# Optimization experiments

Hardware: AMD Instinct MI355X
Metric: run time of the kernel (lower is better)

The kernel has to match this reference:

```python
import jax, jax.numpy as jnp
import numpy as np

B, T, S = 4, 4096, 4096
D_MODEL = 512        # d_query = d_value_in = d_key_in
N_HEADS = 8
D_KEY = 512
D_VALUE = 512
N_OMEGA = 64
EPS = 1e-9
DK_H = D_KEY // N_HEADS      # 64
DV_H = D_VALUE // N_HEADS    # 64


def _glorot(key, shape):
    fan_in, fan_out = shape[-2], shape[-1]
    lim = np.sqrt(6.0 / (fan_in + fan_out))
    return jax.random.uniform(key, shape, jnp.float32, -lim, lim)


def _draw_omega(key, d_feature, n_omega):
    # n_omega == d_feature here -> single orthogonal block scaled by sqrt(d)
    g = jax.random.normal(key, (d_feature, d_feature), jnp.float32)
    q, _ = jnp.linalg.qr(g)
    q = q * jnp.sqrt(jnp.float32(d_feature))
    return q[:n_omega]


def setup_inputs() -> dict:
    key = jax.random.key(0)
    ks = jax.random.split(key, 7)
    return {
        "query": 0.5 * jax.random.normal(ks[0], (B, T, D_MODEL), jnp.float32),
        "value": 0.5 * jax.random.normal(ks[1], (B, S, D_MODEL), jnp.float32),
        "key": 0.5 * jax.random.normal(ks[2], (B, S, D_MODEL), jnp.float32),
        "wq": _glorot(ks[3], (N_HEADS, D_MODEL, DK_H)),
        "wv": _glorot(ks[4], (N_HEADS, D_MODEL, DV_H)),
        "wk": _glorot(ks[5], (N_HEADS, D_MODEL, DK_H)),
        "omega": _draw_omega(ks[6], DK_H, N_OMEGA),
    }


def _phi(x, omega):
    # x: (B,H,T,dk_h) -> (B,H,T,2*n_omega) FAVOR+ positive random features
    square_sum = 0.5 * jnp.sum(x * x, axis=-1, keepdims=True)
    xw = jnp.einsum('bhtk,mk->bhtm', x, omega)
    un = jnp.exp(jnp.concatenate([xw, -xw], axis=-1) - square_sum) + EPS
    return un / jnp.sqrt(jnp.float32(2.0 * N_OMEGA))


def reference(query, value, key, wq, wv, wk, omega):
    q = jnp.einsum('btf,hfk->bhtk', query, wq)   # (B,H,T,dk_h)
    v = jnp.einsum('bsd,hdk->bhsk', value, wv)   # (B,H,S,dv_h)
    k = jnp.einsum('bsf,hfk->bhsk', key, wk)     # (B,H,S,dk_h)
    qp = _phi(q, omega)                          # (B,H,T,2M)
    kp = _phi(k, omega)                          # (B,H,S,2M)
    v1 = jnp.concatenate([v, jnp.ones(v.shape[:-1] + (1,), v.dtype)], axis=-1)
    kv = jnp.einsum('bhsm,bhsd->bhmd', kp, v1)   # (B,H,2M,dv_h+1)
    qkv = jnp.einsum('bhtm,bhmd->bhtd', qp, kv)  # (B,H,T,dv_h+1)
    normalizer = qkv[..., -1:]
    out = qkv[..., :-1] / normalizer
    # faithful to original: plain reshape (B,H,T,dv_h) -> (B,T,D_VALUE), no transpose
    return jnp.reshape(out, (B, T, D_VALUE))
```

## Files before the change

### kernel.cpp

```cpp
#include <hip/hip_runtime.h>

typedef _Float16 half8 __attribute__((ext_vector_type(8)));
typedef _Float16 half4_t __attribute__((ext_vector_type(4)));
typedef short short8 __attribute__((ext_vector_type(8)));
typedef unsigned short u16x4 __attribute__((ext_vector_type(4)));
typedef float f32x4 __attribute__((ext_vector_type(4)));

#define NH 8

__device__ __forceinline__ unsigned short f2bf(float x) {
  union { float f; unsigned u; } v; v.f = x;
  unsigned r = v.u + 0x7FFFu + ((v.u >> 16) & 1u);
  return (unsigned short)(r >> 16);
}

#define DRAIN_BAR()                                  \
  asm volatile("s_waitcnt lgkmcnt(0)" ::: "memory"); \
  __builtin_amdgcn_s_barrier();                      \
  __builtin_amdgcn_sched_barrier(0)

__global__ __launch_bounds__(256) void k0_qk(
    const float* __restrict__ wq, const float* __restrict__ wk,
    const float* __restrict__ omega,
    _Float16* __restrict__ wxq, _Float16* __restrict__ wxk) {
  const int bid = blockIdx.x;
  const int arr = bid >> 7;
  const int h = (bid >> 4) & 7;
  const int ft = (bid >> 1) & 7;
  const int os = bid & 1;
  const int f = threadIdx.x & 63;
  const int w = threadIdx.x >> 6;
  const float* wsrc = (arr ? wk : wq) + ((size_t)h * 512 + ft * 64 + f) * 64;
  float wreg[64];
#pragma unroll
  for (int i = 0; i < 16; ++i) {
    float4 v = *(const float4*)(wsrc + i * 4);
    wreg[i * 4] = v.x; wreg[i * 4 + 1] = v.y; wreg[i * 4 + 2] = v.z; wreg[i * 4 + 3] = v.w;
  }
  _Float16* outp = arr ? wxk : wxq;
  const int k8 = f >> 3, e = f & 7;
#pragma unroll 1
  for (int oo = 0; oo < 8; ++oo) {
    const int o = w * 16 + os * 8 + oo;
    const float* om = omega + o * 64;
    float s = 0.f;
#pragma unroll
    for (int k = 0; k < 64; ++k) s = fmaf(wreg[k], om[k], s);
    outp[((((size_t)h * 8 + ft) * 8 + k8) * 64 + o) * 8 + e] = (_Float16)s;
  }
}

__global__ __launch_bounds__(256) void k0_v(
    const float* __restrict__ wv, _Float16* __restrict__ wvt) {
  int idx = blockIdx.x * 256 + threadIdx.x;
  int h = idx >> 15, o = (idx >> 9) & 63, f = idx & 511;
  float val = wv[((size_t)h * 512 + f) * 64 + o];
  wvt[((((size_t)h * 8 + (f >> 6)) * 8 + ((f >> 3) & 7)) * 64 + o) * 8 + (f & 7)] = (_Float16)val;
}

__global__ __launch_bounds__(512, 1) void fused_kv(
    const float* __restrict__ key, const float* __restrict__ value,
    const _Float16* __restrict__ wxk, const _Float16* __restrict__ wvt,
    float* __restrict__ kvpart) {
  __shared__ __align__(16) _Float16 A[2][128][72];
  __shared__ __align__(16) _Float16 W[2][2][4096];
  __shared__ __align__(16) unsigned short kpT[128][136];
  __shared__ __align__(16) unsigned short vT[64][136];
  const int bid = blockIdx.x;
  const int hp = bid >> 6;
  const int b = (bid >> 4) & 3;
  const int sc = bid & 15;
  const int s0 = sc * 256;
  const int tid = threadIdx.x;
  const int w = tid >> 6;
  const int lane = tid & 63;
  const int g = lane >> 4, c = lane & 15;
  const int hh = w >> 2;
  const int rq = w & 3;
  const int xr = lane >> 4;
  const int xc = (lane & 15) * 4;

  const _Float16* wkb0 = wxk + (size_t)(hp * 2) * 32768;
  const _Float16* wkb1 = wkb0 + 32768;
  const _Float16* wvb0 = wvt + (size_t)(hp * 2) * 32768;
  const _Float16* wvb1 = wvb0 + 32768;

  short8 bones;
#pragma unroll
  for (int i = 0; i < 8; ++i) bones[i] = (c == 0) ? (short)0x3F80 : (short)0;

  f32x4 acc_kv[2][5];
#pragma unroll
  for (int h2 = 0; h2 < 2; ++h2)
#pragma unroll
    for (int j = 0; j < 5; ++j) acc_kv[h2][j] = (f32x4){0.f, 0.f, 0.f, 0.f};

  u16x4 kps[2][4], kms[2][4], vs_[2][4];

  float4 xv[4];
  half8 wr0, wr1;

#pragma unroll 1
  for (int p = 0; p < 4; ++p) {
    const float* xb = ((p & 1) ? value : key) +
                      (size_t)(b * 4096 + s0 + (p >> 1) * 128 + w * 16 + xr) * 512 + xc;
    const _Float16* wb0 = (p & 1) ? wvb0 : wkb0;
    const _Float16* wb1 = (p & 1) ? wvb1 : wkb1;

#pragma unroll
    for (int i = 0; i < 4; ++i) xv[i] = *(const float4*)(xb + i * 2048);
    wr0 = *(const half8*)(wb0 + tid * 8);
    wr1 = *(const half8*)(wb1 + tid * 8);
#pragma unroll
    for (int i = 0; i < 4; ++i) {
      float vv[4] = {xv[i].x, xv[i].y, xv[i].z, xv[i].w};
      half4_t hv;
#pragma unroll
      for (int j2 = 0; j2 < 4; ++j2) hv[j2] = (_Float16)vv[j2];
      *(half4_t*)&A[0][w * 16 + i * 4 + xr][xc] = hv;
    }
    *(half8*)&W[0][0][tid * 8] = wr0;
    *(half8*)&W[0][1][tid * 8] = wr1;
#pragma unroll
    for (int i = 0; i < 4; ++i) xv[i] = *(const float4*)(xb + 64 + i * 2048);
    wr0 = *(const half8*)(wb0 + 4096 + tid * 8);
    wr1 = *(const half8*)(wb1 + 4096 + tid * 8);
    DRAIN_BAR();

    f32x4 accp[2][4];
#pragma unroll
    for (int mf = 0; mf < 2; ++mf)
#pragma unroll
      for (int j = 0; j < 4; ++j) accp[mf][j] = (f32x4){0.f, 0.f, 0.f, 0.f};

#pragma unroll 1
    for (int kc = 0; kc < 8; ++kc) {
      const int cur = kc & 1;
      if (kc < 7) {
        const int nxt = cur ^ 1;
#pragma unroll
        for (int i = 0; i < 4; ++i) {
          float vv[4] = {xv[i].x, xv[i].y, xv[i].z, xv[i].w};
          half4_t hv;
#pragma unroll
          for (int j2 = 0; j2 < 4; ++j2) hv[j2] = (_Float16)vv[j2];
          *(half4_t*)&A[nxt][w * 16 + i * 4 + xr][xc] = hv;
        }
        *(half8*)&W[nxt][0][tid * 8] = wr0;
        *(half8*)&W[nxt][1][tid * 8] = wr1;
        if (kc < 6) {
#pragma unroll
          for (int i = 0; i < 4; ++i)
            xv[i] = *(const float4*)(xb + (kc + 2) * 64 + i * 2048);
          wr0 = *(const half8*)(wb0 + (kc + 2) * 4096 + tid * 8);
          wr1 = *(const half8*)(wb1 + (kc + 2) * 4096 + tid * 8);
        }
      }
#pragma unroll
      for (int ks = 0; ks < 2; ++ks) {
        half8 af0 = *(const half8*)&A[cur][rq * 32 + c][ks * 32 + g * 8];
        half8 af1 = *(const half8*)&A[cur][rq * 32 + 16 + c][ks * 32 + g * 8];
#pragma unroll
        for (int nf = 0; nf < 4; ++nf) {
          half8 wf = *(const half8*)&W[cur][hh][((ks * 4 + g) * 64 + nf * 16 + c) * 8];
          accp[0][nf] = __builtin_amdgcn_mfma_f32_16x16x32_f16(af0, wf, accp[0][nf], 0, 0, 0);
          accp[1][nf] = __builtin_amdgcn_mfma_f32_16x16x32_f16(af1, wf, accp[1][nf], 0, 0, 0);
        }
      }
      DRAIN_BAR();
    }

    if ((p & 1) == 0) {
#pragma unroll
      for (int mf = 0; mf < 2; ++mf) {
        float ss_[4];
#pragma unroll
        for (int j = 0; j < 4; ++j) {
          float s = 0.f;
#pragma unroll
          for (int nf = 0; nf < 4; ++nf) { float q = accp[mf][nf][j]; s = fmaf(q, q, s); }
          s += __shfl_xor(s, 1); s += __shfl_xor(s, 2);
          s += __shfl_xor(s, 4); s += __shfl_xor(s, 8);
          ss_[j] = s * 0.0078125f;
        }
#pragma unroll
        for (int nf = 0; nf < 4; ++nf) {
          u16x4 kp_p, kp_m;
#pragma unroll
          for (int j = 0; j < 4; ++j) {
            float v = accp[mf][nf][j];
            kp_p[j] = f2bf(__expf(v - ss_[j]) + 1e-9f);
            kp_m[j] = f2bf(__expf(-v - ss_[j]) + 1e-9f);
          }
          kps[mf][nf] = kp_p;
          kms[mf][nf] = kp_m;
        }
      }
    } else {
#pragma unroll
      for (int mf = 0; mf < 2; ++mf)
#pragma unroll
        for (int nf = 0; nf < 4; ++nf) {
          u16x4 vv;
#pragma unroll
          for (int j = 0; j < 4; ++j) vv[j] = f2bf(accp[mf][nf][j]);
          vs_[mf][nf] = vv;
        }
#pragma unroll
      for (int h2 = 0; h2 < 2; ++h2) {
        if (hh == h2) {
#pragma unroll
          for (int mf = 0; mf < 2; ++mf)
#pragma unroll
            for (int nf = 0; nf < 4; ++nf) {
              const int m = nf * 16 + c;
              const int sl = rq * 32 + mf * 16 + g * 4;
              *(u16x4*)&kpT[m][sl] = kps[mf][nf];
              *(u16x4*)&kpT[64 + m][sl] = kms[mf][nf];
              *(u16x4*)&vT[m][sl] = vs_[mf][nf];
            }
        }
        DRAIN_BAR();
#pragma unroll
        for (int ks = 0; ks < 4; ++ks) {
          short8 a = *(const short8*)&kpT[w * 16 + c][ks * 32 + g * 8];
#pragma unroll
          for (int nf = 0; nf < 4; ++nf) {
            short8 bb = *(const short8*)&vT[nf * 16 + c][ks * 32 + g * 8];
            acc_kv[h2][nf] = __builtin_amdgcn_mfma_f32_16x16x32_bf16(a, bb, acc_kv[h2][nf], 0, 0, 0);
          }
          acc_kv[h2][4] = __builtin_amdgcn_mfma_f32_16x16x32_bf16(a, bones, acc_kv[h2][4], 0, 0, 0);
        }
        __builtin_amdgcn_s_barrier();
      }
    }
  }

#pragma unroll
  for (int h2 = 0; h2 < 2; ++h2) {
    float* pbase = kvpart + ((size_t)sc * 32 + b * 8 + hp * 2 + h2) * 10240;
#pragma unroll
    for (int nf = 0; nf < 5; ++nf)
#pragma unroll
      for (int j = 0; j < 4; ++j)
        pbase[(w * 16 + g * 4 + j) * 80 + nf * 16 + c] = acc_kv[h2][nf][j];
  }
}

__global__ __launch_bounds__(128) void k3a_denom(
    const float* __restrict__ kvpart, float* __restrict__ invbuf,
    float* __restrict__ lsc) {
  const int bh = blockIdx.x;
  const int m = threadIdx.x;
  const float* base = kvpart + (size_t)bh * 10240 + m * 80 + 64;
  float s = 0.f;
#pragma unroll
  for (int kk = 0; kk < 16; ++kk) s += base[(size_t)kk * 327680];
  invbuf[bh * 128 + m] = 1.0f / s;
  lsc[bh * 128 + m] = __logf(s);
}

__global__ __launch_bounds__(256) void k3b_reduce(
    const float* __restrict__ kvpart, const float* __restrict__ invbuf,
    _Float16* __restrict__ kvnt) {
  const int bh = blockIdx.x;
  const int e0 = blockIdx.y * 1024 + threadIdx.x * 4;
  const int m = e0 / 80;
  const int d0 = e0 - m * 80;
  const float* base = kvpart + (size_t)bh * 10240 + e0;
  f32x4 s = (f32x4){0.f, 0.f, 0.f, 0.f};
#pragma unroll
  for (int kk = 0; kk < 16; ++kk) {
    f32x4 v = *(const f32x4*)(base + (size_t)kk * 327680);
    s += v;
  }
  const float inv = invbuf[bh * 128 + m];
  const int mst = ((m & 63) << 1) | (m >> 6);
  _Float16* outb = kvnt + (size_t)bh * 10240 + mst;
#pragma unroll
  for (int j = 0; j < 4; ++j) {
    const int d = d0 + j;
    float val;
    if (d < 64) val = s[j] * inv;
    else if (d == 64) val = 1.0f;
    else val = 0.f;
    outb[d * 128] = (_Float16)val;
  }
}

__global__ __launch_bounds__(512, 1) void fused_qo(
    const float* __restrict__ query, const _Float16* __restrict__ wxq,
    const _Float16* __restrict__ kvnt, const float* __restrict__ lsc,
    float* __restrict__ out) {
  __shared__ __align__(16) _Float16 A[2][128][72];
  __shared__ __align__(16) _Float16 W[2][2][4096];
  __shared__ __align__(16) _Float16 qpT[128][136];
  const int bid = blockIdx.x;
  const int hp = bid >> 7;
  const int rt = bid & 127;
  const int b = rt >> 5;
  const int t0 = (rt & 31) * 128;
  const int tid = threadIdx.x;
  const int w = tid >> 6;
  const int lane = tid & 63;
  const int g = lane >> 4, c = lane & 15;
  const int hh = w >> 2;
  const int rq = w & 3;
  const int xr = lane >> 4;
  const int xc = (lane & 15) * 4;

  const float* xb = query + (size_t)(rt * 128 + w * 16 + xr) * 512 + xc;
  const _Float16* wb0 = wxq + (size_t)(hp * 2) * 32768;
  const _Float16* wb1 = wb0 + 32768;

  float4 xv[4];
  half8 wr0, wr1;
#pragma unroll
  for (int i = 0; i < 4; ++i) xv[i] = *(const float4*)(xb + i * 2048);
  wr0 = *(const half8*)(wb0 + tid * 8);
  wr1 = *(const half8*)(wb1 + tid * 8);
#pragma unroll
  for (int i = 0; i < 4; ++i) {
    float vv[4] = {xv[i].x, xv[i].y, xv[i].z, xv[i].w};
    half4_t hv;
#pragma unroll
    for (int j2 = 0; j2 < 4; ++j2) hv[j2] = (_Float16)vv[j2];
    *(half4_t*)&A[0][w * 16 + i * 4 + xr][xc] = hv;
  }
  *(half8*)&W[0][0][tid * 8] = wr0;
  *(half8*)&W[0][1][tid * 8] = wr1;
#pragma unroll
  for (int i = 0; i < 4; ++i) xv[i] = *(const float4*)(xb + 64 + i * 2048);
  wr0 = *(const half8*)(wb0 + 4096 + tid * 8);
  wr1 = *(const half8*)(wb1 + 4096 + tid * 8);
  DRAIN_BAR();

  f32x4 accp[2][4];
#pragma unroll
  for (int mf = 0; mf < 2; ++mf)
#pragma unroll
    for (int j = 0; j < 4; ++j) accp[mf][j] = (f32x4){0.f, 0.f, 0.f, 0.f};

#pragma unroll 1
  for (int kc = 0; kc < 8; ++kc) {
    const int cur = kc & 1;
    if (kc < 7) {
      const int nxt = cur ^ 1;
#pragma unroll
      for (int i = 0; i < 4; ++i) {
        float vv[4] = {xv[i].x, xv[i].y, xv[i].z, xv[i].w};
        half4_t hv;
#pragma unroll
        for (int j2 = 0; j2 < 4; ++j2) hv[j2] = (_Float16)vv[j2];
        *(half4_t*)&A[nxt][w * 16 + i * 4 + xr][xc] = hv;
      }
      *(half8*)&W[nxt][0][tid * 8] = wr0;
      *(half8*)&W[nxt][1][tid * 8] = wr1;
      if (kc < 6) {
#pragma unroll
        for (int i = 0; i < 4; ++i)
          xv[i] = *(const float4*)(xb + (kc + 2) * 64 + i * 2048);
        wr0 = *(const half8*)(wb0 + (kc + 2) * 4096 + tid * 8);
        wr1 = *(const half8*)(wb1 + (kc + 2) * 4096 + tid * 8);
      }
    }
#pragma unroll
    for (int ks = 0; ks < 2; ++ks) {
      half8 af0 = *(const half8*)&A[cur][rq * 32 + c][ks * 32 + g * 8];
      half8 af1 = *(const half8*)&A[cur][rq * 32 + 16 + c][ks * 32 + g * 8];
#pragma unroll
      for (int nf = 0; nf < 4; ++nf) {
        half8 wf = *(const half8*)&W[cur][hh][((ks * 4 + g) * 64 + nf * 16 + c) * 8];
        accp[0][nf] = __builtin_amdgcn_mfma_f32_16x16x32_f16(af0, wf, accp[0][nf], 0, 0, 0);
        accp[1][nf] = __builtin_amdgcn_mfma_f32_16x16x32_f16(af1, wf, accp[1][nf], 0, 0, 0);
      }
    }
    DRAIN_BAR();
  }

#pragma unroll
  for (int h2 = 0; h2 < 2; ++h2) {
    const int bh = b * 8 + hp * 2 + h2;
    if (hh == h2) {
      float Lp[4], Lm[4];
#pragma unroll
      for (int nf = 0; nf < 4; ++nf) {
        Lp[nf] = lsc[bh * 128 + nf * 16 + c];
        Lm[nf] = lsc[bh * 128 + 64 + nf * 16 + c];
      }
#pragma unroll
      for (int mf = 0; mf < 2; ++mf) {
        float ss_[4], cm_[4];
#pragma unroll
        for (int j = 0; j < 4; ++j) {
          float s = 0.f;
#pragma unroll
          for (int nf = 0; nf < 4; ++nf) { float q = accp[mf][nf][j]; s = fmaf(q, q, s); }
          s += __shfl_xor(s, 1); s += __shfl_xor(s, 2);
          s += __shfl_xor(s, 4); s += __shfl_xor(s, 8);
          ss_[j] = s * 0.0078125f;
        }
#pragma unroll
        for (int j = 0; j < 4; ++j) {
          float m0 = -1e30f;
#pragma unroll
          for (int nf = 0; nf < 4; ++nf) {
            float v = accp[mf][nf][j];
            m0 = fmaxf(m0, fmaxf(v - ss_[j] + Lp[nf], -v - ss_[j] + Lm[nf]));
            m0 = fmaxf(m0, fmaxf(Lp[nf], Lm[nf]) - 20.723265f);
          }
          m0 = fmaxf(m0, __shfl_xor(m0, 1)); m0 = fmaxf(m0, __shfl_xor(m0, 2));
          m0 = fmaxf(m0, __shfl_xor(m0, 4)); m0 = fmaxf(m0, __shfl_xor(m0, 8));
          cm_[j] = m0;
        }
#pragma unroll
        for (int nf = 0; nf < 4; ++nf) {
          const int m = nf * 16 + c;
#pragma unroll
          for (int j = 0; j < 4; ++j) {
            float v = accp[mf][nf][j];
            _Float16 pp = (_Float16)(__expf(v - ss_[j] + Lp[nf] - cm_[j]) +
                                     1e-9f * __expf(Lp[nf] - cm_[j]));
            _Float16 pm = (_Float16)(__expf(-v - ss_[j] + Lm[nf] - cm_[j]) +
                                     1e-9f * __expf(Lm[nf] - cm_[j]));
            union { unsigned u; _Float16 hhx[2]; } pk;
            pk.hhx[0] = pp; pk.hhx[1] = pm;
            *(unsigned*)&qpT[rq * 32 + mf * 16 + g * 4 + j][2 * m] = pk.u;
          }
        }
      }
    }
    DRAIN_BAR();
    f32x4 acco[5];
#pragma unroll
    for (int j = 0; j < 5; ++j) acco[j] = (f32x4){0.f, 0.f, 0.f, 0.f};
    const _Float16* kvb = kvnt + (size_t)bh * 10240;
#pragma unroll
    for (int ks = 0; ks < 4; ++ks) {
      half8 a = *(const half8*)&qpT[w * 16 + c][ks * 32 + g * 8];
#pragma unroll
      for (int nf = 0; nf < 5; ++nf) {
        half8 bb = *(const half8*)(kvb + (size_t)(nf * 16 + c) * 128 + ks * 32 + g * 8);
        acco[nf] = __builtin_amdgcn_mfma_f32_16x16x32_f16(a, bb, acco[nf], 0, 0, 0);
      }
    }
    const int tb = t0 + w * 16 + g * 4;
#pragma unroll
    for (int j = 0; j < 4; ++j) {
      float nrm = __shfl(acco[4][j], (lane & 48));
      float invn = 1.0f / nrm;
#pragma unroll
      for (int nf = 0; nf < 4; ++nf) {
        out[((size_t)bh * 4096 + tb + j) * 64 + nf * 16 + c] = acco[nf][j] * invn;
      }
    }
    __builtin_amdgcn_s_barrier();
  }
}

extern "C" void kernel_launch(void* const* d_in, const int* in_sizes, int n_in,
                              void* d_out, int out_size, void* d_ws, size_t ws_size,
                              hipStream_t stream) {
  const float* query = (const float*)d_in[0];
  const float* value = (const float*)d_in[1];
  const float* key   = (const float*)d_in[2];
  const float* wq    = (const float*)d_in[3];
  const float* wv    = (const float*)d_in[4];
  const float* wk    = (const float*)d_in[5];
  const float* omega = (const float*)d_in[6];
  float* out = (float*)d_out;
  char* ws = (char*)d_ws;

  _Float16* wxq  = (_Float16*)(ws);
  _Float16* wxk  = (_Float16*)(ws + 524288);
  _Float16* wvt  = (_Float16*)(ws + 1048576);
  float* kvpart  = (float*)(ws + 1572864);
  _Float16* kvnt = (_Float16*)(ws + 22544384);
  float* lsc     = (float*)(ws + 23199744);
  float* invbuf  = (float*)(ws + 23216128);

  k0_qk<<<256, 256, 0, stream>>>(wq, wk, omega, wxq, wxk);
  k0_v<<<1024, 256, 0, stream>>>(wv, wvt);
  fused_kv<<<256, 512, 0, stream>>>(key, value, wxk, wvt, kvpart);
  k3a_denom<<<32, 128, 0, stream>>>(kvpart, invbuf, lsc);
  k3b_reduce<<<dim3(32, 10), 256, 0, stream>>>(kvpart, invbuf, kvnt);
  fused_qo<<<512, 512, 0, stream>>>(query, wxq, kvnt, lsc, out);
}
```

Baseline: 115.8 us.

## Restructure fused_qo into smaller single-head blocks for higher occupancy

```diff
diff --git a/kernel.cpp b/kernel.cpp
--- a/kernel.cpp
+++ b/kernel.cpp
@@ -288,173 +288,141 @@
   }
 }
 
-__global__ __launch_bounds__(512, 1) void fused_qo(
+__global__ __launch_bounds__(256, 4) void fused_qo(
     const float* __restrict__ query, const _Float16* __restrict__ wxq,
     const _Float16* __restrict__ kvnt, const float* __restrict__ lsc,
     float* __restrict__ out) {
-  __shared__ __align__(16) _Float16 A[2][128][72];
-  __shared__ __align__(16) _Float16 W[2][2][4096];
-  __shared__ __align__(16) _Float16 qpT[128][136];
+  __shared__ __align__(16) _Float16 A[64][72];
+  __shared__ __align__(16) _Float16 W[4096];
+  __shared__ __align__(16) _Float16 qpT[64][136];
   const int bid = blockIdx.x;
-  const int hp = bid >> 7;
-  const int rt = bid & 127;
-  const int b = rt >> 5;
-  const int t0 = (rt & 31) * 128;
+  const int h = bid >> 8;
+  const int rt = bid & 255;
+  const int R0 = rt * 64;
+  const int b = R0 >> 12;
+  const int t0 = R0 & 4095;
+  const int bh = b * NH + h;
   const int tid = threadIdx.x;
   const int w = tid >> 6;
   const int lane = tid & 63;
   const int g = lane >> 4, c = lane & 15;
-  const int hh = w >> 2;
-  const int rq = w & 3;
-  const int xr = lane >> 4;
-  const int xc = (lane & 15) * 4;
-
-  const float* xb = query + (size_t)(rt * 128 + w * 16 + xr) * 512 + xc;
-  const _Float16* wb0 = wxq + (size_t)(hp * 2) * 32768;
-  const _Float16* wb1 = wb0 + 32768;
+  const int srow = tid >> 2;
+  const int scol = (tid & 3) * 16;
+
+  const float* xb = query + (size_t)(R0 + srow) * 512 + scol;
+  const _Float16* wb = wxq + (size_t)h * 32768;
 
   float4 xv[4];
   half8 wr0, wr1;
 #pragma unroll
-  for (int i = 0; i < 4; ++i) xv[i] = *(const float4*)(xb + i * 2048);
-  wr0 = *(const half8*)(wb0 + tid * 8);
-  wr1 = *(const half8*)(wb1 + tid * 8);
-#pragma unroll
-  for (int i = 0; i < 4; ++i) {
-    float vv[4] = {xv[i].x, xv[i].y, xv[i].z, xv[i].w};
-    half4_t hv;
-#pragma unroll
-    for (int j2 = 0; j2 < 4; ++j2) hv[j2] = (_Float16)vv[j2];
-    *(half4_t*)&A[0][w * 16 + i * 4 + xr][xc] = hv;
-  }
-  *(half8*)&W[0][0][tid * 8] = wr0;
-  *(half8*)&W[0][1][tid * 8] = wr1;
-#pragma unroll
-  for (int i = 0; i < 4; ++i) xv[i] = *(const float4*)(xb + 64 + i * 2048);
-  wr0 = *(const half8*)(wb0 + 4096 + tid * 8);
-  wr1 = *(const half8*)(wb1 + 4096 + tid * 8);
-  DRAIN_BAR();
-
-  f32x4 accp[2][4];
-#pragma unroll
-  for (int mf = 0; mf < 2; ++mf)
-#pragma unroll
-    for (int j = 0; j < 4; ++j) accp[mf][j] = (f32x4){0.f, 0.f, 0.f, 0.f};
+  for (int i = 0; i < 4; ++i) xv[i] = *(const float4*)(xb + i * 4);
+  wr0 = *(const half8*)(wb + tid * 8);
+  wr1 = *(const half8*)(wb + 2048 + tid * 8);
+
+  f32x4 accp[4];
+#pragma unroll
+  for (int j = 0; j < 4; ++j) accp[j] = (f32x4){0.f, 0.f, 0.f, 0.f};
 
 #pragma unroll 1
   for (int kc = 0; kc < 8; ++kc) {
-    const int cur = kc & 1;
+    DRAIN_BAR();
+#pragma unroll
+    for (int i = 0; i < 4; ++i) {
+      float vv[4] = {xv[i].x, xv[i].y, xv[i].z, xv[i].w};
+      half4_t hv;
+#pragma unroll
+      for (int j2 = 0; j2 < 4; ++j2) hv[j2] = (_Float16)vv[j2];
+      *(half4_t*)&A[srow][scol + i * 4] = hv;
+    }
+    *(half8*)&W[tid * 8] = wr0;
+    *(half8*)&W[2048 + tid * 8] = wr1;
     if (kc < 7) {
-      const int nxt = cur ^ 1;
-#pragma unroll
-      for (int i = 0; i < 4; ++i) {
-        float vv[4] = {xv[i].x, xv[i].y, xv[i].z, xv[i].w};
-        half4_t hv;
-#pragma unroll
-        for (int j2 = 0; j2 < 4; ++j2) hv[j2] = (_Float16)vv[j2];
-        *(half4_t*)&A[nxt][w * 16 + i * 4 + xr][xc] = hv;
+#pragma unroll
+      for (int i = 0; i < 4; ++i)
+        xv[i] = *(const float4*)(xb + (kc + 1) * 64 + i * 4);
+      wr0 = *(const half8*)(wb + (size_t)(kc + 1) * 4096 + tid * 8);
+      wr1 = *(const half8*)(wb + (size_t)(kc + 1) * 4096 + 2048 + tid * 8);
+    }
+    DRAIN_BAR();
+#pragma unroll
+    for (int ks = 0; ks < 2; ++ks) {
+      half8 a = *(const half8*)&A[w * 16 + c][ks * 32 + g * 8];
+#pragma unroll
+      for (int nf = 0; nf < 4; ++nf) {
+        half8 wf = *(const half8*)&W[((ks * 4 + g) * 64 + nf * 16 + c) * 8];
+        accp[nf] = __builtin_amdgcn_mfma_f32_16x16x32_f16(a, wf, accp[nf], 0, 0, 0);
       }
-      *(half8*)&W[nxt][0][tid * 8] = wr0;
-      *(half8*)&W[nxt][1][tid * 8] = wr1;
-      if (kc < 6) {
-#pragma unroll
-        for (int i = 0; i < 4; ++i)
-          xv[i] = *(const float4*)(xb + (kc + 2) * 64 + i * 2048);
-        wr0 = *(const half8*)(wb0 + (kc + 2) * 4096 + tid * 8);
-        wr1 = *(const half8*)(wb1 + (kc + 2) * 4096 + tid * 8);
-      }
-    }
-#pragma unroll
-    for (int ks = 0; ks < 2; ++ks) {
-      half8 af0 = *(const half8*)&A[cur][rq * 32 + c][ks * 32 + g * 8];
-      half8 af1 = *(const half8*)&A[cur][rq * 32 + 16 + c][ks * 32 + g * 8];
-#pragma unroll
-      for (int nf = 0; nf < 4; ++nf) {
-        half8 wf = *(const half8*)&W[cur][hh][((ks * 4 + g) * 64 + nf * 16 + c) * 8];
-        accp[0][nf] = __builtin_amdgcn_mfma_f32_16x16x32_f16(af0, wf, accp[0][nf], 0, 0, 0);
-        accp[1][nf] = __builtin_amdgcn_mfma_f32_16x16x32_f16(af1, wf, accp[1][nf], 0, 0, 0);
-      }
-    }
-    DRAIN_BAR();
-  }
-
-#pragma unroll
-  for (int h2 = 0; h2 < 2; ++h2) {
-    const int bh = b * 8 + hp * 2 + h2;
-    if (hh == h2) {
-      float Lp[4], Lm[4];
-#pragma unroll
-      for (int nf = 0; nf < 4; ++nf) {
-        Lp[nf] = lsc[bh * 128 + nf * 16 + c];
-        Lm[nf] = lsc[bh * 128 + 64 + nf * 16 + c];
-      }
-#pragma unroll
-      for (int mf = 0; mf < 2; ++mf) {
-        float ss_[4], cm_[4];
-#pragma unroll
-        for (int j = 0; j < 4; ++j) {
-          float s = 0.f;
-#pragma unroll
-          for (int nf = 0; nf < 4; ++nf) { float q = accp[mf][nf][j]; s = fmaf(q, q, s); }
-          s += __shfl_xor(s, 1); s += __shfl_xor(s, 2);
-          s += __shfl_xor(s, 4); s += __shfl_xor(s, 8);
-          ss_[j] = s * 0.0078125f;
-        }
-#pragma unroll
-        for (int j = 0; j < 4; ++j) {
-          float m0 = -1e30f;
-#pragma unroll
-          for (int nf = 0; nf < 4; ++nf) {
-            float v = accp[mf][nf][j];
-            m0 = fmaxf(m0, fmaxf(v - ss_[j] + Lp[nf], -v - ss_[j] + Lm[nf]));
-            m0 = fmaxf(m0, fmaxf(Lp[nf], Lm[nf]) - 20.723265f);
-          }
-          m0 = fmaxf(m0, __shfl_xor(m0, 1)); m0 = fmaxf(m0, __shfl_xor(m0, 2));
-          m0 = fmaxf(m0, __shfl_xor(m0, 4)); m0 = fmaxf(m0, __shfl_xor(m0, 8));
-          cm_[j] = m0;
-        }
-#pragma unroll
-        for (int nf = 0; nf < 4; ++nf) {
-          const int m = nf * 16 + c;
-#pragma unroll
-          for (int j = 0; j < 4; ++j) {
-            float v = accp[mf][nf][j];
-            _Float16 pp = (_Float16)(__expf(v - ss_[j] + Lp[nf] - cm_[j]) +
-                                     1e-9f * __expf(Lp[nf] - cm_[j]));
-            _Float16 pm = (_Float16)(__expf(-v - ss_[j] + Lm[nf] - cm_[j]) +
-                                     1e-9f * __expf(Lm[nf] - cm_[j]));
-            union { unsigned u; _Float16 hhx[2]; } pk;
-            pk.hhx[0] = pp; pk.hhx[1] = pm;
-            *(unsigned*)&qpT[rq * 32 + mf * 16 + g * 4 + j][2 * m] = pk.u;
-          }
-        }
-      }
-    }
-    DRAIN_BAR();
-    f32x4 acco[5];
-#pragma unroll
-    for (int j = 0; j < 5; ++j) acco[j] = (f32x4){0.f, 0.f, 0.f, 0.f};
-    const _Float16* kvb = kvnt + (size_t)bh * 10240;
-#pragma unroll
-    for (int ks = 0; ks < 4; ++ks) {
-      half8 a = *(const half8*)&qpT[w * 16 + c][ks * 32 + g * 8];
-#pragma unroll
-      for (int nf = 0; nf < 5; ++nf) {
-        half8 bb = *(const half8*)(kvb + (size_t)(nf * 16 + c) * 128 + ks * 32 + g * 8);
-        acco[nf] = __builtin_amdgcn_mfma_f32_16x16x32_f16(a, bb, acco[nf], 0, 0, 0);
-      }
-    }
-    const int tb = t0 + w * 16 + g * 4;
+    }
+  }
+
+  float Lp[4], Lm[4];
+#pragma unroll
+  for (int nf = 0; nf < 4; ++nf) {
+    Lp[nf] = lsc[bh * 128 + nf * 16 + c];
+    Lm[nf] = lsc[bh * 128 + 64 + nf * 16 + c];
+  }
+  float ss_[4], cm_[4];
+#pragma unroll
+  for (int j = 0; j < 4; ++j) {
+    float s = 0.f;
+#pragma unroll
+    for (int nf = 0; nf < 4; ++nf) { float q = accp[nf][j]; s = fmaf(q, q, s); }
+    s += __shfl_xor(s, 1); s += __shfl_xor(s, 2);
+    s += __shfl_xor(s, 4); s += __shfl_xor(s, 8);
+    ss_[j] = s * 0.0078125f;
+  }
+#pragma unroll
+  for (int j = 0; j < 4; ++j) {
+    float m0 = -1e30f;
+#pragma unroll
+    for (int nf = 0; nf < 4; ++nf) {
+      float v = accp[nf][j];
+      m0 = fmaxf(m0, fmaxf(v - ss_[j] + Lp[nf], -v - ss_[j] + Lm[nf]));
+      m0 = fmaxf(m0, fmaxf(Lp[nf], Lm[nf]) - 20.723265f);
+    }
+    m0 = fmaxf(m0, __shfl_xor(m0, 1)); m0 = fmaxf(m0, __shfl_xor(m0, 2));
+    m0 = fmaxf(m0, __shfl_xor(m0, 4)); m0 = fmaxf(m0, __shfl_xor(m0, 8));
+    cm_[j] = m0;
+  }
+#pragma unroll
+  for (int nf = 0; nf < 4; ++nf) {
+    const int m = nf * 16 + c;
 #pragma unroll
     for (int j = 0; j < 4; ++j) {
-      float nrm = __shfl(acco[4][j], (lane & 48));
-      float invn = 1.0f / nrm;
-#pragma unroll
-      for (int nf = 0; nf < 4; ++nf) {
-        out[((size_t)bh * 4096 + tb + j) * 64 + nf * 16 + c] = acco[nf][j] * invn;
-      }
-    }
-    __builtin_amdgcn_s_barrier();
+      float v = accp[nf][j];
+      _Float16 pp = (_Float16)(__expf(v - ss_[j] + Lp[nf] - cm_[j]) +
+                               1e-9f * __expf(Lp[nf] - cm_[j]));
+      _Float16 pm = (_Float16)(__expf(-v - ss_[j] + Lm[nf] - cm_[j]) +
+                               1e-9f * __expf(Lm[nf] - cm_[j]));
+      union { unsigned u; _Float16 hh[2]; } pk;
+      pk.hh[0] = pp; pk.hh[1] = pm;
+      *(unsigned*)&qpT[w * 16 + g * 4 + j][2 * m] = pk.u;
+    }
+  }
+  DRAIN_BAR();
+
+  f32x4 acco[5];
+#pragma unroll
+  for (int j = 0; j < 5; ++j) acco[j] = (f32x4){0.f, 0.f, 0.f, 0.f};
+  const _Float16* kvb = kvnt + (size_t)bh * 10240;
+#pragma unroll
+  for (int ks = 0; ks < 4; ++ks) {
+    half8 a = *(const half8*)&qpT[w * 16 + c][ks * 32 + g * 8];
+#pragma unroll
+    for (int nf = 0; nf < 5; ++nf) {
+      half8 bb = *(const half8*)(kvb + (size_t)(nf * 16 + c) * 128 + ks * 32 + g * 8);
+      acco[nf] = __builtin_amdgcn_mfma_f32_16x16x32_f16(a, bb, acco[nf], 0, 0, 0);
+    }
+  }
+  const int tb = t0 + w * 16 + g * 4;
+#pragma unroll
+  for (int j = 0; j < 4; ++j) {
+    float nrm = __shfl(acco[4][j], (lane & 48));
+    float invn = 1.0f / nrm;
+#pragma unroll
+    for (int nf = 0; nf < 4; ++nf) {
+      out[((size_t)bh * 4096 + tb + j) * 64 + nf * 16 + c] = acco[nf][j] * invn;
+    }
   }
 }
 
@@ -484,5 +452,5 @@
   fused_kv<<<256, 512, 0, stream>>>(key, value, wxk, wvt, kvpart);
   k3a_denom<<<32, 128, 0, stream>>>(kvpart, invbuf, lsc);
   k3b_reduce<<<dim3(32, 10), 256, 0, stream>>>(kvpart, invbuf, kvnt);
-  fused_qo<<<512, 512, 0, stream>>>(query, wxq, kvnt, lsc, out);
-}
+  fused_qo<<<2048, 256, 0, stream>>>(query, wxq, kvnt, lsc, out);
+}
```

Result: faster. 110.0 us (-5.0%).

## Retile fused_qo to one head per block with 256-row tiles and resident weights

Applied to the files above, without the earlier changes.

```diff
diff --git a/kernel.cpp b/kernel.cpp
--- a/kernel.cpp
+++ b/kernel.cpp
@@ -292,85 +292,79 @@
     const float* __restrict__ query, const _Float16* __restrict__ wxq,
     const _Float16* __restrict__ kvnt, const float* __restrict__ lsc,
     float* __restrict__ out) {
-  __shared__ __align__(16) _Float16 A[2][128][72];
-  __shared__ __align__(16) _Float16 W[2][2][4096];
-  __shared__ __align__(16) _Float16 qpT[128][136];
+  __shared__ __align__(16) _Float16 A[2][256][72];
+  __shared__ __align__(16) _Float16 W[8][4096];
   const int bid = blockIdx.x;
-  const int hp = bid >> 7;
-  const int rt = bid & 127;
-  const int b = rt >> 5;
-  const int t0 = (rt & 31) * 128;
+  const int h = bid >> 6;
+  const int b = (bid >> 4) & 3;
+  const int tt = bid & 15;
+  const int t0 = tt * 256;
   const int tid = threadIdx.x;
   const int w = tid >> 6;
   const int lane = tid & 63;
   const int g = lane >> 4, c = lane & 15;
-  const int hh = w >> 2;
-  const int rq = w & 3;
   const int xr = lane >> 4;
   const int xc = (lane & 15) * 4;
-
-  const float* xb = query + (size_t)(rt * 128 + w * 16 + xr) * 512 + xc;
-  const _Float16* wb0 = wxq + (size_t)(hp * 2) * 32768;
-  const _Float16* wb1 = wb0 + 32768;
-
-  float4 xv[4];
-  half8 wr0, wr1;
-#pragma unroll
-  for (int i = 0; i < 4; ++i) xv[i] = *(const float4*)(xb + i * 2048);
-  wr0 = *(const half8*)(wb0 + tid * 8);
-  wr1 = *(const half8*)(wb1 + tid * 8);
-#pragma unroll
-  for (int i = 0; i < 4; ++i) {
-    float vv[4] = {xv[i].x, xv[i].y, xv[i].z, xv[i].w};
-    half4_t hv;
-#pragma unroll
-    for (int j2 = 0; j2 < 4; ++j2) hv[j2] = (_Float16)vv[j2];
-    *(half4_t*)&A[0][w * 16 + i * 4 + xr][xc] = hv;
-  }
-  *(half8*)&W[0][0][tid * 8] = wr0;
-  *(half8*)&W[0][1][tid * 8] = wr1;
-#pragma unroll
-  for (int i = 0; i < 4; ++i) xv[i] = *(const float4*)(xb + 64 + i * 2048);
-  wr0 = *(const half8*)(wb0 + 4096 + tid * 8);
-  wr1 = *(const half8*)(wb1 + 4096 + tid * 8);
+  const int bh = b * NH + h;
+
+  const float* xb = query + (size_t)(b * 4096 + t0 + w * 32 + xr) * 512 + xc;
+  const _Float16* wb = wxq + (size_t)h * 32768;
+
+  f32x4 accp[2][4];
+#pragma unroll
+  for (int mf = 0; mf < 2; ++mf)
+#pragma unroll
+    for (int j = 0; j < 4; ++j) accp[mf][j] = (f32x4){0.f, 0.f, 0.f, 0.f};
+
+  float4 xv[8];
+
+  {
+    half8 wr[8];
+#pragma unroll
+    for (int s = 0; s < 8; ++s) wr[s] = *(const half8*)(wb + (size_t)s * 4096 + tid * 8);
+#pragma unroll
+    for (int i = 0; i < 8; ++i) xv[i] = *(const float4*)(xb + i * 2048);
+#pragma unroll
+    for (int s = 0; s < 8; ++s) *(half8*)&W[s][tid * 8] = wr[s];
+#pragma unroll
+    for (int i = 0; i < 8; ++i) {
+      float vv[4] = {xv[i].x, xv[i].y, xv[i].z, xv[i].w};
+      half4_t hv;
+#pragma unroll
+      for (int j2 = 0; j2 < 4; ++j2) hv[j2] = (_Float16)vv[j2];
+      *(half4_t*)&A[0][w * 32 + i * 4 + xr][xc] = hv;
+    }
+#pragma unroll
+    for (int i = 0; i < 8; ++i) xv[i] = *(const float4*)(xb + 64 + i * 2048);
+  }
   DRAIN_BAR();
 
-  f32x4 accp[2][4];
-#pragma unroll
-  for (int mf = 0; mf < 2; ++mf)
-#pragma unroll
-    for (int j = 0; j < 4; ++j) accp[mf][j] = (f32x4){0.f, 0.f, 0.f, 0.f};
-
-#pragma unroll 1
+#pragma unroll
   for (int kc = 0; kc < 8; ++kc) {
     const int cur = kc & 1;
     if (kc < 7) {
       const int nxt = cur ^ 1;
 #pragma unroll
-      for (int i = 0; i < 4; ++i) {
+      for (int i = 0; i < 8; ++i) {
         float vv[4] = {xv[i].x, xv[i].y, xv[i].z, xv[i].w};
         half4_t hv;
 #pragma unroll
         for (int j2 = 0; j2 < 4; ++j2) hv[j2] = (_Float16)vv[j2];
-        *(half4_t*)&A[nxt][w * 16 + i * 4 + xr][xc] = hv;
-      }
-      *(half8*)&W[nxt][0][tid * 8] = wr0;
-      *(half8*)&W[nxt][1][tid * 8] = wr1;
+        *(half4_t*)&A[nxt][w * 32 + i * 4 + xr][xc] = hv;
+      }
       if (kc < 6) {
 #pragma unroll
-        for (int i = 0; i < 4; ++i)
+        for (int i = 0; i < 8; ++i)
           xv[i] = *(const float4*)(xb + (kc + 2) * 64 + i * 2048);
-        wr0 = *(const half8*)(wb0 + (kc + 2) * 4096 + tid * 8);
-        wr1 = *(const half8*)(wb1 + (kc + 2) * 4096 + tid * 8);
       }
     }
 #pragma unroll
     for (int ks = 0; ks < 2; ++ks) {
-      half8 af0 = *(const half8*)&A[cur][rq * 32 + c][ks * 32 + g * 8];
-      half8 af1 = *(const half8*)&A[cur][rq * 32 + 16 + c][ks * 32 + g * 8];
+      half8 af0 = *(const half8*)&A[cur][w * 32 + c][ks * 32 + g * 8];
+      half8 af1 = *(const half8*)&A[cur][w * 32 + 16 + c][ks * 32 + g * 8];
 #pragma unroll
       for (int nf = 0; nf < 4; ++nf) {
-        half8 wf = *(const half8*)&W[cur][hh][((ks * 4 + g) * 64 + nf * 16 + c) * 8];
+        half8 wf = *(const half8*)&W[kc][((ks * 4 + g) * 64 + nf * 16 + c) * 8];
         accp[0][nf] = __builtin_amdgcn_mfma_f32_16x16x32_f16(af0, wf, accp[0][nf], 0, 0, 0);
         accp[1][nf] = __builtin_amdgcn_mfma_f32_16x16x32_f16(af1, wf, accp[1][nf], 0, 0, 0);
       }
@@ -378,73 +372,73 @@
     DRAIN_BAR();
   }
 
-#pragma unroll
-  for (int h2 = 0; h2 < 2; ++h2) {
-    const int bh = b * 8 + hp * 2 + h2;
-    if (hh == h2) {
-      float Lp[4], Lm[4];
+  _Float16* qpT = &A[0][0][0];
+
+  float Lp[4], Lm[4];
+#pragma unroll
+  for (int nf = 0; nf < 4; ++nf) {
+    Lp[nf] = lsc[bh * 128 + nf * 16 + c];
+    Lm[nf] = lsc[bh * 128 + 64 + nf * 16 + c];
+  }
+#pragma unroll
+  for (int mf = 0; mf < 2; ++mf) {
+    float ss_[4], cm_[4];
+#pragma unroll
+    for (int j = 0; j < 4; ++j) {
+      float s = 0.f;
+#pragma unroll
+      for (int nf = 0; nf < 4; ++nf) { float q = accp[mf][nf][j]; s = fmaf(q, q, s); }
+      s += __shfl_xor(s, 1); s += __shfl_xor(s, 2);
+      s += __shfl_xor(s, 4); s += __shfl_xor(s, 8);
+      ss_[j] = s * 0.0078125f;
+    }
+#pragma unroll
+    for (int j = 0; j < 4; ++j) {
+      float m0 = -1e30f;
 #pragma unroll
       for (int nf = 0; nf < 4; ++nf) {
-        Lp[nf] = lsc[bh * 128 + nf * 16 + c];
-        Lm[nf] = lsc[bh * 128 + 64 + nf * 16 + c];
-      }
-#pragma unroll
-      for (int mf = 0; mf < 2; ++mf) {
-        float ss_[4], cm_[4];
-#pragma unroll
-        for (int j = 0; j < 4; ++j) {
-          float s = 0.f;
-#pragma unroll
-          for (int nf = 0; nf < 4; ++nf) { float q = accp[mf][nf][j]; s = fmaf(q, q, s); }
-          s += __shfl_xor(s, 1); s += __shfl_xor(s, 2);
-          s += __shfl_xor(s, 4); s += __shfl_xor(s, 8);
-          ss_[j] = s * 0.0078125f;
-        }
-#pragma unroll
-        for (int j = 0; j < 4; ++j) {
-          float m0 = -1e30f;
-#pragma unroll
-          for (int nf = 0; nf < 4; ++nf) {
-            float v = accp[mf][nf][j];
-            m0 = fmaxf(m0, fmaxf(v - ss_[j] + Lp[nf], -v - ss_[j] + Lm[nf]));
-            m0 = fmaxf(m0, fmaxf(Lp[nf], Lm[nf]) - 20.723265f);
-          }
-          m0 = fmaxf(m0, __shfl_xor(m0, 1)); m0 = fmaxf(m0, __shfl_xor(m0, 2));
-          m0 = fmaxf(m0, __shfl_xor(m0, 4)); m0 = fmaxf(m0, __shfl_xor(m0, 8));
-          cm_[j] = m0;
-        }
-#pragma unroll
-        for (int nf = 0; nf < 4; ++nf) {
-          const int m = nf * 16 + c;
-#pragma unroll
-          for (int j = 0; j < 4; ++j) {
-            float v = accp[mf][nf][j];
-            _Float16 pp = (_Float16)(__expf(v - ss_[j] + Lp[nf] - cm_[j]) +
-                                     1e-9f * __expf(Lp[nf] - cm_[j]));
-            _Float16 pm = (_Float16)(__expf(-v - ss_[j] + Lm[nf] - cm_[j]) +
-                                     1e-9f * __expf(Lm[nf] - cm_[j]));
-            union { unsigned u; _Float16 hhx[2]; } pk;
-            pk.hhx[0] = pp; pk.hhx[1] = pm;
-            *(unsigned*)&qpT[rq * 32 + mf * 16 + g * 4 + j][2 * m] = pk.u;
-          }
-        }
-      }
-    }
-    DRAIN_BAR();
+        float v = accp[mf][nf][j];
+        m0 = fmaxf(m0, fmaxf(v - ss_[j] + Lp[nf], -v - ss_[j] + Lm[nf]));
+        m0 = fmaxf(m0, fmaxf(Lp[nf], Lm[nf]) - 20.723265f);
+      }
+      m0 = fmaxf(m0, __shfl_xor(m0, 1)); m0 = fmaxf(m0, __shfl_xor(m0, 2));
+      m0 = fmaxf(m0, __shfl_xor(m0, 4)); m0 = fmaxf(m0, __shfl_xor(m0, 8));
+      cm_[j] = m0;
+    }
+#pragma unroll
+    for (int nf = 0; nf < 4; ++nf) {
+      const int m = nf * 16 + c;
+#pragma unroll
+      for (int j = 0; j < 4; ++j) {
+        float v = accp[mf][nf][j];
+        _Float16 pp = (_Float16)(__expf(v - ss_[j] + Lp[nf] - cm_[j]) +
+                                 1e-9f * __expf(Lp[nf] - cm_[j]));
+        _Float16 pm = (_Float16)(__expf(-v - ss_[j] + Lm[nf] - cm_[j]) +
+                                 1e-9f * __expf(Lm[nf] - cm_[j]));
+        union { unsigned u; _Float16 hh_[2]; } pk;
+        pk.hh_[0] = pp; pk.hh_[1] = pm;
+        *(unsigned*)&qpT[(size_t)(w * 32 + mf * 16 + g * 4 + j) * 136 + 2 * m] = pk.u;
+      }
+    }
+  }
+  DRAIN_BAR();
+
+  const _Float16* kvb = kvnt + (size_t)bh * 10240;
+#pragma unroll
+  for (int mf = 0; mf < 2; ++mf) {
     f32x4 acco[5];
 #pragma unroll
     for (int j = 0; j < 5; ++j) acco[j] = (f32x4){0.f, 0.f, 0.f, 0.f};
-    const _Float16* kvb = kvnt + (size_t)bh * 10240;
 #pragma unroll
     for (int ks = 0; ks < 4; ++ks) {
-      half8 a = *(const half8*)&qpT[w * 16 + c][ks * 32 + g * 8];
+      half8 a = *(const half8*)&qpT[(size_t)(w * 32 + mf * 16 + c) * 136 + ks * 32 + g * 8];
 #pragma unroll
       for (int nf = 0; nf < 5; ++nf) {
         half8 bb = *(const half8*)(kvb + (size_t)(nf * 16 + c) * 128 + ks * 32 + g * 8);
         acco[nf] = __builtin_amdgcn_mfma_f32_16x16x32_f16(a, bb, acco[nf], 0, 0, 0);
       }
     }
-    const int tb = t0 + w * 16 + g * 4;
+    const int tb = t0 + w * 32 + mf * 16 + g * 4;
 #pragma unroll
     for (int j = 0; j < 4; ++j) {
       float nrm = __shfl(acco[4][j], (lane & 48));
@@ -454,7 +448,6 @@
         out[((size_t)bh * 4096 + tb + j) * 64 + nf * 16 + c] = acco[nf][j] * invn;
       }
     }
-    __builtin_amdgcn_s_barrier();
   }
 }
 
```

Result: no change. 115.9 us (+0.1%).
